# Performance work log

Hardware: AMD Instinct MI355X
Metric: run time of the kernel (lower is better)

The kernel has to match this reference:

```python
import jax, jax.numpy as jnp
import numpy as np

N_NODES = 100000
N_EDGES = 1600000
IN_C = 128
OUT_C = 128


def setup_inputs() -> dict:
    key = jax.random.key(0)
    k1, k2, k3, k4 = jax.random.split(key, 4)
    x = jax.random.normal(k1, (N_NODES, IN_C), dtype=jnp.float32)
    W = jax.random.normal(k2, (IN_C, OUT_C), dtype=jnp.float32) * (1.0 / np.sqrt(IN_C))
    b = jax.random.normal(k3, (OUT_C,), dtype=jnp.float32) * 0.02
    edge_index = jax.random.randint(k4, (2, N_EDGES), 0, N_NODES, dtype=jnp.int32)
    return {"x": x, "W": W, "b": b, "edge_index": edge_index}


def reference(x, W, b, edge_index):
    N = x.shape[0]
    # Symmetrize edges: concat(edge_index, flip(edge_index)) as in adj()
    row = jnp.concatenate([edge_index[0], edge_index[1]])  # [2E]
    col = jnp.concatenate([edge_index[1], edge_index[0]])  # [2E]
    w = jnp.ones(row.shape, dtype=x.dtype)
    # gcn_norm with self loops (fill value 1): deg includes self-loop weight
    deg = jax.ops.segment_sum(w, row, num_segments=N) + 1.0
    dinv = jnp.where(deg > 0, jax.lax.rsqrt(deg), 0.0)  # [N]
    # Dense linear projection (bias=False)
    xw = x @ W  # [N, out]
    # SpMM: y[row] += dinv[row]*dinv[col] * xw[col]  (scatter-add == coalesced adj matmul)
    norm = dinv[row] * dinv[col]  # [2E]
    msgs = norm[:, None] * xw[col]  # [2E, out] -- dominant memory traffic
    y = jax.ops.segment_sum(msgs, row, num_segments=N)
    # Self-loop contribution: weight dinv[i]^2
    y = y + (dinv * dinv)[:, None] * xw
    return y + b
```

## Files before the change

kernel.cpp:

```cpp
#include <hip/hip_runtime.h>
#include <math.h>

constexpr int N = 100000;
constexpr int E = 1600000;
constexpr int C = 128;
constexpr int NPB   = 256;
constexpr int NBUCK = (N + NPB - 1) / NPB;
constexpr int CAP   = 9472;
constexpr int ADJ_STRIDE = CAP + NPB * 7;

__device__ inline unsigned f2bf(float f) {
    unsigned u = __float_as_uint(f);
    return (u + 0x7fffu + ((u >> 16) & 1u)) >> 16;
}
__device__ inline unsigned pack2(float lo, float hi) {
    return f2bf(lo) | (f2bf(hi) << 16);
}
__device__ inline float bf_lo(unsigned m) { return __uint_as_float(m << 16); }
__device__ inline float bf_hi(unsigned m) { return __uint_as_float(m & 0xffff0000u); }

__global__ __launch_bounds__(256) void k_bin(const int* __restrict__ ei,
                                             int* __restrict__ gcount,
                                             unsigned* __restrict__ staging) {
    __shared__ int cnt[NBUCK];
    __shared__ int wbase[NBUCK];
    const int t = threadIdx.x;
    const long tile = (long)blockIdx.x * 2048;
    for (int i = t; i < NBUCK; i += 256) cnt[i] = 0;
    __syncthreads();
    int b0[8], b1[8], lo0[8], lo1[8];
    unsigned p0[8], p1[8];
    bool val[8];
#pragma unroll
    for (int j = 0; j < 8; ++j) {
        long e = tile + j * 256 + t;
        val[j] = e < E;
        if (val[j]) {
            int u = __builtin_nontemporal_load(ei + e);
            int v = __builtin_nontemporal_load(ei + E + e);
            b0[j] = u >> 8;
            b1[j] = v >> 8;
            p0[j] = ((unsigned)(u & 255) << 17) | (unsigned)v;
            p1[j] = ((unsigned)(v & 255) << 17) | (unsigned)u;
            lo0[j] = atomicAdd(&cnt[b0[j]], 1);
            lo1[j] = atomicAdd(&cnt[b1[j]], 1);
        }
    }
    __syncthreads();
    for (int i = t; i < NBUCK; i += 256) wbase[i] = atomicAdd(&gcount[i], cnt[i]);
    __syncthreads();
#pragma unroll
    for (int j = 0; j < 8; ++j) {
        if (val[j]) {
            staging[(size_t)b0[j] * CAP + wbase[b0[j]] + lo0[j]] = p0[j];
            staging[(size_t)b1[j] * CAP + wbase[b1[j]] + lo1[j]] = p1[j];
        }
    }
}

__global__ __launch_bounds__(512) void k_csr(const unsigned* __restrict__ staging,
                                             const int* __restrict__ gcount,
                                             int* __restrict__ deg,
                                             float* __restrict__ dinv,
                                             int* __restrict__ rowptr,
                                             int* __restrict__ adj) {
    __shared__ int hist[NPB];
    __shared__ int wpart[4];
    const int g = blockIdx.x;
    const int t = threadIdx.x;
    const int lane = t & 63, wid = t >> 6;
    const int cnt = gcount[g];
    int* slice = adj + (size_t)g * ADJ_STRIDE;
    {
        const int4 fill = {N, N, N, N};
        for (int i = t; i < ADJ_STRIDE / 4; i += 512) ((int4*)slice)[i] = fill;
    }
    for (int i = t; i < NPB; i += 512) hist[i] = 0;
    __syncthreads();
    const unsigned* base = staging + (size_t)g * CAP;
    for (int i = t; i < cnt; i += 512) atomicAdd(&hist[base[i] >> 17], 1);
    __syncthreads();
    const int d  = (t < NPB) ? hist[t] : 0;
    const int pd = (d + 7) & ~7;
    int v = pd;
#pragma unroll
    for (int off = 1; off < 64; off <<= 1) {
        int n = __shfl_up(v, off);
        if (lane >= off) v += n;
    }
    if (lane == 63 && wid < 4) wpart[wid] = v;
    __syncthreads();
    if (t == 0) {
        int r = 0;
#pragma unroll
        for (int w = 0; w < 4; ++w) { int x = wpart[w]; wpart[w] = r; r += x; }
    }
    __syncthreads();
    const int pstart = v - pd + ((wid < 4) ? wpart[wid] : 0);
    if (t < NPB) {
        const int node = g * NPB + t;
        if (node < N) {
            deg[node]    = d;
            dinv[node]   = rsqrtf((float)d + 1.0f);
            rowptr[node] = g * ADJ_STRIDE + pstart;
        }
    }
    __syncthreads();
    if (t < NPB) hist[t] = pstart;
    __syncthreads();
    for (int i = t; i < cnt; i += 512) {
        const unsigned e = base[i];
        const int pos = atomicAdd(&hist[e >> 17], 1);
        slice[pos] = (int)(e & 0x1ffffu);
    }
}

__global__ __launch_bounds__(256) void k_gemm(const float* __restrict__ x,
                                              const float* __restrict__ W,
                                              const float* __restrict__ dinv,
                                              unsigned* __restrict__ z_lo,
                                              unsigned* __restrict__ z_hi) {
    __shared__ float Ws[32][128];
    __shared__ float xs[64][33];

    const int t   = threadIdx.x;
    const int r0  = (t & 15) * 4;
    const int c0  = (t >> 4) * 8;
    const int bid = blockIdx.x;

    float acc[4][8];
#pragma unroll
    for (int i = 0; i < 4; ++i)
#pragma unroll
        for (int j = 0; j < 8; ++j) acc[i][j] = 0.0f;

    const int lrow = t >> 2;
    const int lk   = (t & 3) * 8;
    const long grow = (long)bid * 64 + lrow;
    const bool rvalid = grow < N;

    for (int k0 = 0; k0 < C; k0 += 32) {
        const float4* Wg = (const float4*)(W + (size_t)k0 * C);
        float4* Wsv = (float4*)(&Ws[0][0]);
#pragma unroll
        for (int j = 0; j < 4; ++j) Wsv[t + 256 * j] = Wg[t + 256 * j];
        float4 a0 = {0, 0, 0, 0}, a1 = {0, 0, 0, 0};
        if (rvalid) {
            a0 = *(const float4*)(x + grow * C + k0 + lk);
            a1 = *(const float4*)(x + grow * C + k0 + lk + 4);
        }
        xs[lrow][lk + 0] = a0.x; xs[lrow][lk + 1] = a0.y;
        xs[lrow][lk + 2] = a0.z; xs[lrow][lk + 3] = a0.w;
        xs[lrow][lk + 4] = a1.x; xs[lrow][lk + 5] = a1.y;
        xs[lrow][lk + 6] = a1.z; xs[lrow][lk + 7] = a1.w;
        __syncthreads();

#pragma unroll 8
        for (int k = 0; k < 32; ++k) {
            float4 w0 = *(const float4*)&Ws[k][c0];
            float4 w1 = *(const float4*)&Ws[k][c0 + 4];
            float xv[4];
#pragma unroll
            for (int i = 0; i < 4; ++i) xv[i] = xs[r0 + i][k];
#pragma unroll
            for (int i = 0; i < 4; ++i) {
                acc[i][0] = fmaf(xv[i], w0.x, acc[i][0]);
                acc[i][1] = fmaf(xv[i], w0.y, acc[i][1]);
                acc[i][2] = fmaf(xv[i], w0.z, acc[i][2]);
                acc[i][3] = fmaf(xv[i], w0.w, acc[i][3]);
                acc[i][4] = fmaf(xv[i], w1.x, acc[i][4]);
                acc[i][5] = fmaf(xv[i], w1.y, acc[i][5]);
                acc[i][6] = fmaf(xv[i], w1.z, acc[i][6]);
                acc[i][7] = fmaf(xv[i], w1.w, acc[i][7]);
            }
        }
        __syncthreads();
    }

    unsigned* zh = (c0 < 64) ? z_lo : z_hi;
    const int ch = (c0 & 63) >> 1;
#pragma unroll
    for (int i = 0; i < 4; ++i) {
        long r = (long)bid * 64 + r0 + i;
        if (r >= N) break;
        const float dv = dinv[r];
        uint4 pk = {pack2(dv * acc[i][0], dv * acc[i][1]), pack2(dv * acc[i][2], dv * acc[i][3]),
                    pack2(dv * acc[i][4], dv * acc[i][5]), pack2(dv * acc[i][6], dv * acc[i][7])};
        *(uint4*)(zh + r * 32 + ch) = pk;
    }
}

__global__ __launch_bounds__(256) void k_gather(const int* __restrict__ rowptr,
                                                const int* __restrict__ deg,
                                                const float* __restrict__ dinv,
                                                const int* __restrict__ adj,
                                                const unsigned* __restrict__ z_lo,
                                                const unsigned* __restrict__ z_hi,
                                                const float* __restrict__ b,
                                                float* __restrict__ out,
                                                int nb_h) {
    const int half = (blockIdx.x >= nb_h) ? 1 : 0;
    const int u = (blockIdx.x - half * nb_h) * 4 + (threadIdx.x >> 6);
    if (u >= N) return;
    const int lane = threadIdx.x & 63;
    const int h = lane >> 5;
    const int c = lane & 31;
    const int d  = __builtin_amdgcn_readfirstlane(deg[u]);
    const int pd = (d + 7) & ~7;
    const int st = __builtin_amdgcn_readfirstlane(rowptr[u]);
    const float du = dinv[u];
    const unsigned* zh = (half ? z_hi : z_lo) + c;

    float ax, ay;
    {
        const unsigned ms = (h == 0) ? zh[(size_t)(unsigned)u << 5] : 0u;
        ax = bf_lo(ms); ay = bf_hi(ms);
    }

#define RL(i) __builtin_amdgcn_readlane(v, (i))
#define LDP(P) (zh[(size_t)(unsigned)(h ? RL(2 * (P) + 1) : RL(2 * (P))) << 5])
#define ACC(m) { ax += bf_lo(m); ay += bf_hi(m); }

    for (int j0 = 0; j0 < pd; j0 += 64) {
        const int cntc = min(64, pd - j0);
        int v = 0;
        if (lane < cntc) v = adj[st + j0 + lane];
        const int np = cntc >> 1;
        unsigned m0 = LDP(0), m1 = LDP(1), m2 = LDP(2), m3 = LDP(3);
        for (int p = 4; p < np; p += 4) {
            unsigned n0 = LDP(p), n1 = LDP(p + 1), n2 = LDP(p + 2), n3 = LDP(p + 3);
            ACC(m0); ACC(m1); ACC(m2); ACC(m3);
            m0 = n0; m1 = n1; m2 = n2; m3 = n3;
        }
        ACC(m0); ACC(m1); ACC(m2); ACC(m3);
    }
#undef RL
#undef LDP
#undef ACC

    ax += __shfl_xor(ax, 32);
    ay += __shfl_xor(ay, 32);

    if (h == 0) {
        const float* bh = b + 64 * half + 2 * c;
        const float2 bb = {bh[0], bh[1]};
        float2 o = {fmaf(du, ax, bb.x), fmaf(du, ay, bb.y)};
        *(float2*)(out + (size_t)u * C + 64 * half + 2 * c) = o;
    }
}

extern "C" void kernel_launch(void* const* d_in, const int* in_sizes, int n_in,
                              void* d_out, int out_size, void* d_ws, size_t ws_size,
                              hipStream_t stream) {
    const float* x  = (const float*)d_in[0];
    const float* W  = (const float*)d_in[1];
    const float* b  = (const float*)d_in[2];
    const int*   ei = (const int*)d_in[3];
    float* out = (float*)d_out;

    char* p = (char*)d_ws;
    unsigned* zbase = (unsigned*)p;
    unsigned* z_lo = zbase;
    unsigned* z_hi = zbase + (size_t)(N + 1) * 32;
    unsigned* staging = zbase;
    p += (size_t)2 * (N + 1) * 32 * sizeof(unsigned);
    int* adj = (int*)p;             p += (size_t)NBUCK * ADJ_STRIDE * sizeof(int);
    int* deg = (int*)p;             p += (size_t)N * sizeof(int);
    float* dinv = (float*)p;        p += (size_t)N * sizeof(float);
    int* rowptr = (int*)p;          p += (size_t)(N + 4) * sizeof(int);
    int* gcount = (int*)p;          p += 512 * sizeof(int);

    hipMemsetAsync(gcount, 0, 512 * sizeof(int), stream);
    k_bin<<<(E + 2047) / 2048, 256, 0, stream>>>(ei, gcount, staging);
    k_csr<<<NBUCK, 512, 0, stream>>>(staging, gcount, deg, dinv, rowptr, adj);
    hipMemsetAsync(z_lo + (size_t)N * 32, 0, 128, stream);
    hipMemsetAsync(z_hi + (size_t)N * 32, 0, 128, stream);
    k_gemm<<<(N + 63) / 64, 256, 0, stream>>>(x, W, dinv, z_lo, z_hi);
    const int nb_h = (N + 3) / 4;
    k_gather<<<2 * nb_h, 256, 0, stream>>>(rowptr, deg, dinv, adj, z_lo, z_hi, b, out, nb_h);
}
```

Baseline: 333.1 us.

## Use split-bf16 MFMA GEMM and gather full 128-channel rows per wavefront

The FP32 SIMT GEMM is replaced by an MFMA bf16 GEMM. It splits x and W into hi and lo bf16 parts and sums three products, which keeps close to FP32 accuracy. A new small kernel pre-splits and transposes W, and also zeroes the padding row. The z buffer goes from two 64-channel halves to one interleaved 128-channel row layout, so the gather kernel uses one wavefront per node over all channels with 8-deep unrolled loads, instead of two half-launches. This aims to cut GEMM compute time and to halve the adjacency reads and index broadcasts in the gather, at the cost of an extra launch and the approximation error of the split.

After: 339.6 us. No clear change (+2.0%).

```diff
diff --git a/kernel.cpp b/kernel.cpp
--- a/kernel.cpp
+++ b/kernel.cpp
@@ -8,6 +8,9 @@
 constexpr int NBUCK = (N + NPB - 1) / NPB;
 constexpr int CAP   = 9472;
 constexpr int ADJ_STRIDE = CAP + NPB * 7;
+
+typedef __attribute__((ext_vector_type(8))) short bf16x8;
+typedef __attribute__((ext_vector_type(4))) float f32x4;
 
 __device__ inline unsigned f2bf(float f) {
     unsigned u = __float_as_uint(f);
@@ -115,78 +118,91 @@
     }
 }
 
+__global__ __launch_bounds__(256) void k_wsplit(const float* __restrict__ W,
+                                                unsigned short* __restrict__ WhiT,
+                                                unsigned short* __restrict__ WloT,
+                                                unsigned* __restrict__ z16) {
+    const int i = blockIdx.x * 256 + threadIdx.x;
+    if (i < C * C) {
+        const int k = i >> 7, c = i & 127;
+        const float f = W[i];
+        const unsigned hb = f2bf(f);
+        const float hf = __uint_as_float(hb << 16);
+        WhiT[c * 128 + k] = (unsigned short)hb;
+        WloT[c * 128 + k] = (unsigned short)f2bf(f - hf);
+    }
+    if (blockIdx.x == 0 && threadIdx.x < 64) z16[(size_t)N * 64 + threadIdx.x] = 0u;
+}
+
 __global__ __launch_bounds__(256) void k_gemm(const float* __restrict__ x,
-                                              const float* __restrict__ W,
+                                              const unsigned short* __restrict__ WhiT,
+                                              const unsigned short* __restrict__ WloT,
                                               const float* __restrict__ dinv,
-                                              unsigned* __restrict__ z_lo,
-                                              unsigned* __restrict__ z_hi) {
-    __shared__ float Ws[32][128];
-    __shared__ float xs[64][33];
-
-    const int t   = threadIdx.x;
-    const int r0  = (t & 15) * 4;
-    const int c0  = (t >> 4) * 8;
+                                              unsigned* __restrict__ z16) {
+    __shared__ unsigned short xh[64][136];
+    __shared__ unsigned short xl[64][136];
+    const int t = threadIdx.x;
     const int bid = blockIdx.x;
 
-    float acc[4][8];
-#pragma unroll
-    for (int i = 0; i < 4; ++i)
-#pragma unroll
-        for (int j = 0; j < 8; ++j) acc[i][j] = 0.0f;
-
-    const int lrow = t >> 2;
-    const int lk   = (t & 3) * 8;
-    const long grow = (long)bid * 64 + lrow;
-    const bool rvalid = grow < N;
-
-    for (int k0 = 0; k0 < C; k0 += 32) {
-        const float4* Wg = (const float4*)(W + (size_t)k0 * C);
-        float4* Wsv = (float4*)(&Ws[0][0]);
-#pragma unroll
-        for (int j = 0; j < 4; ++j) Wsv[t + 256 * j] = Wg[t + 256 * j];
-        float4 a0 = {0, 0, 0, 0}, a1 = {0, 0, 0, 0};
-        if (rvalid) {
-            a0 = *(const float4*)(x + grow * C + k0 + lk);
-            a1 = *(const float4*)(x + grow * C + k0 + lk + 4);
-        }
-        xs[lrow][lk + 0] = a0.x; xs[lrow][lk + 1] = a0.y;
-        xs[lrow][lk + 2] = a0.z; xs[lrow][lk + 3] = a0.w;
-        xs[lrow][lk + 4] = a1.x; xs[lrow][lk + 5] = a1.y;
-        xs[lrow][lk + 6] = a1.z; xs[lrow][lk + 7] = a1.w;
-        __syncthreads();
-
-#pragma unroll 8
-        for (int k = 0; k < 32; ++k) {
-            float4 w0 = *(const float4*)&Ws[k][c0];
-            float4 w1 = *(const float4*)&Ws[k][c0 + 4];
-            float xv[4];
-#pragma unroll
-            for (int i = 0; i < 4; ++i) xv[i] = xs[r0 + i][k];
-#pragma unroll
-            for (int i = 0; i < 4; ++i) {
-                acc[i][0] = fmaf(xv[i], w0.x, acc[i][0]);
-                acc[i][1] = fmaf(xv[i], w0.y, acc[i][1]);
-                acc[i][2] = fmaf(xv[i], w0.z, acc[i][2]);
-                acc[i][3] = fmaf(xv[i], w0.w, acc[i][3]);
-                acc[i][4] = fmaf(xv[i], w1.x, acc[i][4]);
-                acc[i][5] = fmaf(xv[i], w1.y, acc[i][5]);
-                acc[i][6] = fmaf(xv[i], w1.z, acc[i][6]);
-                acc[i][7] = fmaf(xv[i], w1.w, acc[i][7]);
-            }
-        }
-        __syncthreads();
-    }
-
-    unsigned* zh = (c0 < 64) ? z_lo : z_hi;
-    const int ch = (c0 & 63) >> 1;
-#pragma unroll
-    for (int i = 0; i < 4; ++i) {
-        long r = (long)bid * 64 + r0 + i;
-        if (r >= N) break;
-        const float dv = dinv[r];
-        uint4 pk = {pack2(dv * acc[i][0], dv * acc[i][1]), pack2(dv * acc[i][2], dv * acc[i][3]),
-                    pack2(dv * acc[i][4], dv * acc[i][5]), pack2(dv * acc[i][6], dv * acc[i][7])};
-        *(uint4*)(zh + r * 32 + ch) = pk;
+#pragma unroll
+    for (int j = 0; j < 8; ++j) {
+        const int f4i = j * 256 + t;
+        const int row = f4i >> 5;
+        const int k4  = f4i & 31;
+        const long gr = (long)bid * 64 + row;
+        float4 f = {0.f, 0.f, 0.f, 0.f};
+        if (gr < N) f = *(const float4*)(x + gr * C + k4 * 4);
+        unsigned hq[4], lq[4];
+#pragma unroll
+        for (int e = 0; e < 4; ++e) {
+            const float fe = (&f.x)[e];
+            const unsigned hb = f2bf(fe);
+            hq[e] = hb;
+            lq[e] = f2bf(fe - __uint_as_float(hb << 16));
+        }
+        uint2 ph = {hq[0] | (hq[1] << 16), hq[2] | (hq[3] << 16)};
+        uint2 pl = {lq[0] | (lq[1] << 16), lq[2] | (lq[3] << 16)};
+        *(uint2*)(&xh[row][k4 * 4]) = ph;
+        *(uint2*)(&xl[row][k4 * 4]) = pl;
+    }
+    __syncthreads();
+
+    const int wid = t >> 6, l = t & 63;
+    const int nb = wid * 16;
+    const int lr = l & 15, lg = l >> 4;
+
+    f32x4 acc[8];
+#pragma unroll
+    for (int i = 0; i < 8; ++i) acc[i] = (f32x4){0.f, 0.f, 0.f, 0.f};
+
+    const unsigned short* xhp = &xh[nb + lr][lg * 8];
+    const unsigned short* xlp = &xl[nb + lr][lg * 8];
+
+#pragma unroll
+    for (int kc = 0; kc < 4; ++kc) {
+        const bf16x8 bh = *(const bf16x8*)(xhp + kc * 32);
+        const bf16x8 bl = *(const bf16x8*)(xlp + kc * 32);
+#pragma unroll
+        for (int ct = 0; ct < 8; ++ct) {
+            const int woff = (ct * 16 + lr) * 128 + kc * 32 + lg * 8;
+            const bf16x8 ahi = *(const bf16x8*)(WhiT + woff);
+            const bf16x8 alo = *(const bf16x8*)(WloT + woff);
+            acc[ct] = __builtin_amdgcn_mfma_f32_16x16x32_bf16(ahi, bh, acc[ct], 0, 0, 0);
+            acc[ct] = __builtin_amdgcn_mfma_f32_16x16x32_bf16(ahi, bl, acc[ct], 0, 0, 0);
+            acc[ct] = __builtin_amdgcn_mfma_f32_16x16x32_bf16(alo, bh, acc[ct], 0, 0, 0);
+        }
+    }
+
+    const long node = (long)bid * 64 + nb + lr;
+    if (node < N) {
+        const float dv = dinv[node];
+#pragma unroll
+        for (int ct = 0; ct < 8; ++ct) {
+            const int ch0 = ct * 16 + lg * 4;
+            uint2 pk = {pack2(dv * acc[ct][0], dv * acc[ct][1]),
+                        pack2(dv * acc[ct][2], dv * acc[ct][3])};
+            *(uint2*)(z16 + node * 64 + ch0 / 2) = pk;
+        }
     }
 }
 
@@ -194,59 +210,51 @@
                                                 const int* __restrict__ deg,
                                                 const float* __restrict__ dinv,
                                                 const int* __restrict__ adj,
-                                                const unsigned* __restrict__ z_lo,
-                                                const unsigned* __restrict__ z_hi,
+                                                const unsigned* __restrict__ z16,
                                                 const float* __restrict__ b,
-                                                float* __restrict__ out,
-                                                int nb_h) {
-    const int half = (blockIdx.x >= nb_h) ? 1 : 0;
-    const int u = (blockIdx.x - half * nb_h) * 4 + (threadIdx.x >> 6);
+                                                float* __restrict__ out) {
+    const int u = blockIdx.x * 4 + (threadIdx.x >> 6);
     if (u >= N) return;
     const int lane = threadIdx.x & 63;
-    const int h = lane >> 5;
-    const int c = lane & 31;
     const int d  = __builtin_amdgcn_readfirstlane(deg[u]);
     const int pd = (d + 7) & ~7;
     const int st = __builtin_amdgcn_readfirstlane(rowptr[u]);
     const float du = dinv[u];
-    const unsigned* zh = (half ? z_hi : z_lo) + c;
-
-    float ax, ay;
-    {
-        const unsigned ms = (h == 0) ? zh[(size_t)(unsigned)u << 5] : 0u;
-        ax = bf_lo(ms); ay = bf_hi(ms);
-    }
-
-#define RL(i) __builtin_amdgcn_readlane(v, (i))
-#define LDP(P) (zh[(size_t)(unsigned)(h ? RL(2 * (P) + 1) : RL(2 * (P))) << 5])
-#define ACC(m) { ax += bf_lo(m); ay += bf_hi(m); }
+
+    const unsigned ms = z16[((size_t)(unsigned)u << 6) + lane];
+    float ax = bf_lo(ms), ay = bf_hi(ms);
+
+    unsigned q0, q1, q2, q3, q4, q5, q6, q7;
+    unsigned r0, r1, r2, r3, r4, r5, r6, r7;
+
+#define ZR(j) z16[((size_t)(unsigned)__builtin_amdgcn_readlane(v, (j)) << 6) + lane]
+#define LD8(A, p) A##0 = ZR((p) + 0); A##1 = ZR((p) + 1); A##2 = ZR((p) + 2); \
+                  A##3 = ZR((p) + 3); A##4 = ZR((p) + 4); A##5 = ZR((p) + 5); \
+                  A##6 = ZR((p) + 6); A##7 = ZR((p) + 7);
+#define AC8(A) ax += bf_lo(A##0); ay += bf_hi(A##0); ax += bf_lo(A##1); ay += bf_hi(A##1); \
+               ax += bf_lo(A##2); ay += bf_hi(A##2); ax += bf_lo(A##3); ay += bf_hi(A##3); \
+               ax += bf_lo(A##4); ay += bf_hi(A##4); ax += bf_lo(A##5); ay += bf_hi(A##5); \
+               ax += bf_lo(A##6); ay += bf_hi(A##6); ax += bf_lo(A##7); ay += bf_hi(A##7);
 
     for (int j0 = 0; j0 < pd; j0 += 64) {
         const int cntc = min(64, pd - j0);
-        int v = 0;
-        if (lane < cntc) v = adj[st + j0 + lane];
-        const int np = cntc >> 1;
-        unsigned m0 = LDP(0), m1 = LDP(1), m2 = LDP(2), m3 = LDP(3);
-        for (int p = 4; p < np; p += 4) {
-            unsigned n0 = LDP(p), n1 = LDP(p + 1), n2 = LDP(p + 2), n3 = LDP(p + 3);
-            ACC(m0); ACC(m1); ACC(m2); ACC(m3);
-            m0 = n0; m1 = n1; m2 = n2; m3 = n3;
-        }
-        ACC(m0); ACC(m1); ACC(m2); ACC(m3);
-    }
-#undef RL
-#undef LDP
-#undef ACC
-
-    ax += __shfl_xor(ax, 32);
-    ay += __shfl_xor(ay, 32);
-
-    if (h == 0) {
-        const float* bh = b + 64 * half + 2 * c;
-        const float2 bb = {bh[0], bh[1]};
-        float2 o = {fmaf(du, ax, bb.x), fmaf(du, ay, bb.y)};
-        *(float2*)(out + (size_t)u * C + 64 * half + 2 * c) = o;
-    }
+        const int v = adj[st + j0 + lane];
+        int p = 8;
+        LD8(q, 0);
+        for (; p + 16 <= cntc; p += 16) {
+            LD8(r, p); AC8(q);
+            LD8(q, p + 8); AC8(r);
+        }
+        if (p < cntc) { LD8(r, p); AC8(q); AC8(r); }
+        else          { AC8(q); }
+    }
+#undef ZR
+#undef LD8
+#undef AC8
+
+    const float2 bb = *(const float2*)(b + 2 * lane);
+    float2 o = {fmaf(du, ax, bb.x), fmaf(du, ay, bb.y)};
+    *(float2*)(out + (size_t)u * C + 2 * lane) = o;
 }
 
 extern "C" void kernel_launch(void* const* d_in, const int* in_sizes, int n_in,
@@ -259,23 +267,21 @@
     float* out = (float*)d_out;
 
     char* p = (char*)d_ws;
-    unsigned* zbase = (unsigned*)p;
-    unsigned* z_lo = zbase;
-    unsigned* z_hi = zbase + (size_t)(N + 1) * 32;
-    unsigned* staging = zbase;
-    p += (size_t)2 * (N + 1) * 32 * sizeof(unsigned);
+    unsigned* z16 = (unsigned*)p;
+    unsigned* staging = z16;
+    p += (size_t)(N + 1) * 64 * sizeof(unsigned);
     int* adj = (int*)p;             p += (size_t)NBUCK * ADJ_STRIDE * sizeof(int);
     int* deg = (int*)p;             p += (size_t)N * sizeof(int);
     float* dinv = (float*)p;        p += (size_t)N * sizeof(float);
     int* rowptr = (int*)p;          p += (size_t)(N + 4) * sizeof(int);
     int* gcount = (int*)p;          p += 512 * sizeof(int);
+    unsigned short* WhiT = (unsigned short*)p;  p += (size_t)C * C * sizeof(unsigned short);
+    unsigned short* WloT = (unsigned short*)p;
 
     hipMemsetAsync(gcount, 0, 512 * sizeof(int), stream);
     k_bin<<<(E + 2047) / 2048, 256, 0, stream>>>(ei, gcount, staging);
     k_csr<<<NBUCK, 512, 0, stream>>>(staging, gcount, deg, dinv, rowptr, adj);
-    hipMemsetAsync(z_lo + (size_t)N * 32, 0, 128, stream);
-    hipMemsetAsync(z_hi + (size_t)N * 32, 0, 128, stream);
-    k_gemm<<<(N + 63) / 64, 256, 0, stream>>>(x, W, dinv, z_lo, z_hi);
-    const int nb_h = (N + 3) / 4;
-    k_gather<<<2 * nb_h, 256, 0, stream>>>(rowptr, deg, dinv, adj, z_lo, z_hi, b, out, nb_h);
-}
+    k_wsplit<<<64, 256, 0, stream>>>(W, WhiT, WloT, z16);
+    k_gemm<<<(N + 63) / 64, 256, 0, stream>>>(x, WhiT, WloT, dinv, z16);
+    k_gather<<<(N + 3) / 4, 256, 0, stream>>>(rowptr, deg, dinv, adj, z16, b, out);
+}
```
